# Performance work log

Hardware: AMD Instinct MI355X
Metric: run time of the kernel (lower is better)

Reference implementation:

```python
import jax, jax.numpy as jnp
import numpy as np

B, S, D, H = 2, 2048, 1024, 16
DK = D // H


def setup_inputs() -> dict:
    key = jax.random.key(0)
    ks = jax.random.split(key, 12)
    std = 1.0 / np.sqrt(D)
    inp = {
        "query": jax.random.normal(ks[0], (B, S, D), jnp.float32),
        "key": jax.random.normal(ks[1], (B, S, D), jnp.float32),
        "value": jax.random.normal(ks[2], (B, S, D), jnp.float32),
        # causal decoder mask [B, 1, S, S]; 0 -> masked
        "mask": jnp.broadcast_to(jnp.tril(jnp.ones((S, S), jnp.int32)), (B, 1, S, S)),
        "wq": jax.random.uniform(ks[3], (D, D), jnp.float32, -std, std),
        "bq": jax.random.uniform(ks[4], (D,), jnp.float32, -std, std),
        "wk": jax.random.uniform(ks[5], (D, D), jnp.float32, -std, std),
        "bk": jax.random.uniform(ks[6], (D,), jnp.float32, -std, std),
        "wv": jax.random.uniform(ks[7], (D, D), jnp.float32, -std, std),
        "bv": jax.random.uniform(ks[8], (D,), jnp.float32, -std, std),
        "wo": jax.random.uniform(ks[9], (D, D), jnp.float32, -std, std),
        "bo": jax.random.uniform(ks[10], (D,), jnp.float32, -std, std),
    }
    return inp


def _split_heads(x):
    b, s, _ = x.shape
    return x.reshape(b, s, H, DK).transpose(0, 2, 1, 3)  # [B,H,S,DK]


def reference(query, key, value, mask, wq, bq, wk, bk, wv, bv, wo, bo):
    # nn.Linear: y = x @ W^T + b
    q = _split_heads(query @ wq.T + bq)
    k = _split_heads(key @ wk.T + bk)
    v = _split_heads(value @ wv.T + bv)
    scores = jnp.einsum("bhqd,bhkd->bhqk", q, k) / np.sqrt(DK).astype(np.float32)
    scores = jnp.where(mask == 0, jnp.float32(-1e9), scores)
    attn = jax.nn.softmax(scores, axis=-1)
    # dropout is identity in eval mode
    out = jnp.einsum("bhqk,bhkd->bhqd", attn, v)
    out = out.transpose(0, 2, 1, 3).reshape(query.shape[0], -1, D)
    return out @ wo.T + bo
```

## Files before the change

### kernel.cpp

```cpp
#include <hip/hip_runtime.h>
#include <hip/hip_bf16.h>
#include <cstdint>
#include <cstddef>

#define B_ 2
#define S_ 2048
#define D_ 1024
#define H_ 16
#define DK_ 64

#define AS1 __attribute__((address_space(1)))
#define AS3 __attribute__((address_space(3)))

typedef __attribute__((ext_vector_type(8))) short short8;
typedef __attribute__((ext_vector_type(4))) float f32x4;
typedef __attribute__((ext_vector_type(16))) float f32x16;
typedef __attribute__((ext_vector_type(4))) unsigned short ushort4_t;

__device__ __forceinline__ unsigned short f2bf(float f) {
    union { float f; unsigned u; } x; x.f = f;
    unsigned r = x.u + 0x7fffu + ((x.u >> 16) & 1u);
    return (unsigned short)(r >> 16);
}

__device__ __forceinline__ unsigned pack_bf16(float lo, float hi_) {
    union { __hip_bfloat162 h; unsigned u; } cv;
    cv.h = __float22bfloat162_rn(make_float2(lo, hi_));
    return cv.u;
}

__device__ __forceinline__ float xor32f(float x, int hi) {
#if __has_builtin(__builtin_amdgcn_permlane32_swap)
    unsigned u = __builtin_bit_cast(unsigned, x);
    auto r = __builtin_amdgcn_permlane32_swap(u, u, false, false);
    return __builtin_bit_cast(float, hi ? r[0] : r[1]);
#else
    return __shfl_xor(x, 32);
#endif
}

__device__ __forceinline__ void swap32(unsigned a, unsigned b, unsigned& x, unsigned& y, int hi) {
#if __has_builtin(__builtin_amdgcn_permlane32_swap)
    auto r = __builtin_amdgcn_permlane32_swap(a, b, false, false);
    x = r[0]; y = r[1];
#else
    unsigned pa_ = __shfl_xor(a, 32), pb_ = __shfl_xor(b, 32);
    x = hi ? pb_ : a;
    y = hi ? b : pa_;
#endif
}

__global__ __launch_bounds__(256) void cvt_all(
    const float* __restrict__ q, const float* __restrict__ k, const float* __restrict__ v,
    const float* __restrict__ wq, const float* __restrict__ wk, const float* __restrict__ wv,
    const float* __restrict__ wo,
    unsigned short* __restrict__ xq, unsigned short* __restrict__ xk, unsigned short* __restrict__ xv,
    unsigned short* __restrict__ wqb, unsigned short* __restrict__ wkb, unsigned short* __restrict__ wvb,
    unsigned short* __restrict__ wob) {
    int b = blockIdx.x;
    const float* src; unsigned short* dst; int rel;
    if (b < 6144) {
        int which = b >> 11; rel = b & 2047;
        src = (which == 0) ? q : (which == 1) ? k : v;
        dst = (which == 0) ? xq : (which == 1) ? xk : xv;
    } else {
        int bb = b - 6144; int which = bb >> 9; rel = bb & 511;
        src = (which == 0) ? wq : (which == 1) ? wk : (which == 2) ? wv : wo;
        dst = (which == 0) ? wqb : (which == 1) ? wkb : (which == 2) ? wvb : wob;
    }
    int i = rel * 256 + threadIdx.x;
    const float4* s4 = (const float4*)src;
    float4 a = s4[2 * i], c = s4[2 * i + 1];
    short8 o;
    o[0] = (short)f2bf(a.x); o[1] = (short)f2bf(a.y); o[2] = (short)f2bf(a.z); o[3] = (short)f2bf(a.w);
    o[4] = (short)f2bf(c.x); o[5] = (short)f2bf(c.y); o[6] = (short)f2bf(c.z); o[7] = (short)f2bf(c.w);
    *(short8*)(dst + (size_t)i * 8) = o;
}

template <int OUTMODE>
__device__ __forceinline__ void gemm_body(const unsigned short* __restrict__ Ab,
                                          const unsigned short* __restrict__ Wb,
                                          const float* __restrict__ bias,
                                          void* __restrict__ Cout, float scale,
                                          unsigned short* __restrict__ As0,
                                          unsigned short* __restrict__ As1,
                                          unsigned short* __restrict__ Bs0,
                                          unsigned short* __restrict__ Bs1) {
    constexpr int Kd = 1024;
    const int t = threadIdx.x;
    const int l = t & 63;
    const int l15 = l & 15, l4 = l >> 4;
    const int wid = t >> 6;
    const int wm = wid >> 1, wn = wid & 1;
    const int m0 = (blockIdx.x * 4 + (blockIdx.y & 3)) * 128;
    const int n0 = (blockIdx.y >> 2) * 128;

    f32x4 acc[4][4] = {};

    int ldsoff[4];
    int sgo[4];
#pragma unroll
    for (int p = 0; p < 4; p++) {
        int off = p * 4096 + t * 16;
        int row = off >> 7;
        int slot = (off >> 4) & 7;
        ldsoff[p] = off;
        sgo[p] = row * Kd + (slot ^ (row & 7)) * 8;
    }

#define GLOAD(BUFA, BUFB, K0)                                                         \
    {                                                                                 \
        _Pragma("unroll") for (int p = 0; p < 4; p++)                                 \
            __builtin_amdgcn_global_load_lds(                                         \
                (const AS1 void*)(Ab + (size_t)m0 * Kd + sgo[p] + (K0)),              \
                (AS3 void*)((char*)(BUFA) + ldsoff[p]), 16, 0, 0);                    \
        _Pragma("unroll") for (int p = 0; p < 4; p++)                                 \
            __builtin_amdgcn_global_load_lds(                                         \
                (const AS1 void*)(Wb + (size_t)n0 * Kd + sgo[p] + (K0)),              \
                (AS3 void*)((char*)(BUFB) + ldsoff[p]), 16, 0, 0);                    \
    }

#define GEMMSTEP(CA, CB, NA, NB, K0)                                                  \
    {                                                                                 \
        if ((K0) + 64 < Kd) {                                                         \
            GLOAD(NA, NB, (K0) + 64);                                                 \
            asm volatile("s_waitcnt vmcnt(8)" ::: "memory");                          \
        } else {                                                                      \
            asm volatile("s_waitcnt vmcnt(0)" ::: "memory");                          \
        }                                                                             \
        __builtin_amdgcn_sched_barrier(0);                                            \
        __builtin_amdgcn_s_barrier();                                                 \
        __builtin_amdgcn_sched_barrier(0);                                            \
        _Pragma("unroll") for (int kk = 0; kk < 2; kk++) {                            \
            short8 af[4], bfr[4];                                                     \
            _Pragma("unroll") for (int mi = 0; mi < 4; mi++) {                        \
                int row = wm * 64 + mi * 16 + l15;                                    \
                int slot = kk * 4 + l4;                                               \
                af[mi] = *(const short8*)((const char*)(CA) + row * 128 +             \
                                          ((slot ^ (row & 7)) << 4));                 \
            }                                                                         \
            _Pragma("unroll") for (int ni = 0; ni < 4; ni++) {                        \
                int row = wn * 64 + ni * 16 + l15;                                    \
                int slot = kk * 4 + l4;                                               \
                bfr[ni] = *(const short8*)((const char*)(CB) + row * 128 +            \
                                           ((slot ^ (row & 7)) << 4));                \
            }                                                                         \
            _Pragma("unroll") for (int mi = 0; mi < 4; mi++)                          \
                _Pragma("unroll") for (int ni = 0; ni < 4; ni++)                      \
                    acc[mi][ni] = __builtin_amdgcn_mfma_f32_16x16x32_bf16(            \
                        af[mi], bfr[ni], acc[mi][ni], 0, 0, 0);                       \
        }                                                                             \
        __builtin_amdgcn_s_barrier();                                                 \
        __builtin_amdgcn_sched_barrier(0);                                            \
    }

    GLOAD(As0, Bs0, 0);
    for (int k0 = 0; k0 < Kd; k0 += 128) {
        GEMMSTEP(As0, Bs0, As1, Bs1, k0);
        GEMMSTEP(As1, Bs1, As0, Bs0, k0 + 64);
    }
#undef GEMMSTEP
#undef GLOAD

#pragma unroll
    for (int mi = 0; mi < 4; mi++) {
#pragma unroll
        for (int ni = 0; ni < 4; ni++) {
            int n = n0 + wn * 64 + ni * 16 + l15;
            float bn = bias[n];
            int mb = m0 + wm * 64 + mi * 16 + l4 * 4;
            if constexpr (OUTMODE == 2) {
                int b = mb >> 11, s = mb & 2047, h = n >> 6, dk = n & 63;
                ushort4_t vv;
#pragma unroll
                for (int j = 0; j < 4; j++) vv[j] = f2bf(acc[mi][ni][j] + bn);
                *(ushort4_t*)((unsigned short*)Cout + ((size_t)(b * H_ + h) * DK_ + dk) * S_ + s) = vv;
            } else {
#pragma unroll
                for (int j = 0; j < 4; j++) {
                    float v = (acc[mi][ni][j] + bn) * scale;
                    int m = mb + j;
                    if constexpr (OUTMODE == 0) {
                        int b = m >> 11, s = m & 2047, h = n >> 6, dk = n & 63;
                        ((unsigned short*)Cout)[(((size_t)b * H_ + h) * S_ + s) * DK_ + dk] = f2bf(v);
                    } else {
                        ((float*)Cout)[(size_t)m * D_ + n] = v;
                    }
                }
            }
        }
    }
}

__global__ __launch_bounds__(256, 2) void qkv_gemm(
    const unsigned short* __restrict__ xq, const unsigned short* __restrict__ xk,
    const unsigned short* __restrict__ xv, const unsigned short* __restrict__ wqb,
    const unsigned short* __restrict__ wkb, const unsigned short* __restrict__ wvb,
    const float* __restrict__ bq, const float* __restrict__ bk, const float* __restrict__ bv,
    unsigned short* __restrict__ qo, unsigned short* __restrict__ ko, unsigned short* __restrict__ vto,
    float qscale) {
    __shared__ unsigned short As[2][128 * 64];
    __shared__ unsigned short Bs[2][128 * 64];
    int z = blockIdx.z;
    if (z == 2) {
        gemm_body<2>(xv, wvb, bv, vto, 1.0f, As[0], As[1], Bs[0], Bs[1]);
    } else if (z == 0) {
        gemm_body<0>(xq, wqb, bq, qo, qscale, As[0], As[1], Bs[0], Bs[1]);
    } else {
        gemm_body<0>(xk, wkb, bk, ko, 1.0f, As[0], As[1], Bs[0], Bs[1]);
    }
}

__global__ __launch_bounds__(256, 2) void out_gemm(const unsigned short* __restrict__ Aa,
                                                   const unsigned short* __restrict__ Wo,
                                                   const float* __restrict__ bo,
                                                   float* __restrict__ out) {
    __shared__ unsigned short As[2][128 * 64];
    __shared__ unsigned short Bs[2][128 * 64];
    gemm_body<1>(Aa, Wo, bo, out, 1.0f, As[0], As[1], Bs[0], Bs[1]);
}

union AttnSm {
    unsigned short kv[2][2][128 * 64];
    struct { float obuf[2][2][32][64]; float lArr[2][4][32]; } m;
};

__device__ __forceinline__ void attn_compute(const short8 kf[4], const short8 vf[4],
                                             const short8 qf[4], int lq, int hi, bool diag,
                                             f32x16& o0, f32x16& o1, float& l_run) {
    f32x16 sT = {};
    __builtin_amdgcn_s_setprio(1);
#pragma unroll
    for (int c = 0; c < 4; c++)
        sT = __builtin_amdgcn_mfma_f32_32x32x16_bf16(kf[c], qf[c], sT, 0, 0, 0);
    __builtin_amdgcn_s_setprio(0);

    float e[16];
#pragma unroll
    for (int r = 0; r < 16; r++) e[r] = exp2f(sT[r]);
    if (diag) {
#pragma unroll
        for (int r = 0; r < 16; r++) {
            int kvl = (r & 3) + 8 * (r >> 2) + 4 * hi;
            e[r] = (kvl <= lq) ? e[r] : 0.0f;
        }
    }

    float s8[8];
#pragma unroll
    for (int r = 0; r < 8; r++) s8[r] = e[2 * r] + e[2 * r + 1];
#pragma unroll
    for (int r = 0; r < 4; r++) s8[r] = s8[r] + s8[r + 4];
    float ps = (s8[0] + s8[1]) + (s8[2] + s8[3]);
    ps += xor32f(ps, hi);
    l_run += ps;

    unsigned OW[8];
#pragma unroll
    for (int w = 0; w < 8; w++) OW[w] = pack_bf16(e[2 * w], e[2 * w + 1]);

    union { unsigned u[4]; short8 s; } pa0, pa1;
    swap32(OW[0], OW[2], pa0.u[0], pa0.u[2], hi);
    swap32(OW[1], OW[3], pa0.u[1], pa0.u[3], hi);
    swap32(OW[4], OW[6], pa1.u[0], pa1.u[2], hi);
    swap32(OW[5], OW[7], pa1.u[1], pa1.u[3], hi);

    __builtin_amdgcn_s_setprio(1);
    o0 = __builtin_amdgcn_mfma_f32_32x32x16_bf16(pa0.s, vf[0], o0, 0, 0, 0);
    o1 = __builtin_amdgcn_mfma_f32_32x32x16_bf16(pa0.s, vf[1], o1, 0, 0, 0);
    o0 = __builtin_amdgcn_mfma_f32_32x32x16_bf16(pa1.s, vf[2], o0, 0, 0, 0);
    o1 = __builtin_amdgcn_mfma_f32_32x32x16_bf16(pa1.s, vf[3], o1, 0, 0, 0);
    __builtin_amdgcn_s_setprio(0);
}

__global__ __launch_bounds__(512, 4) void attn_kernel(const unsigned short* __restrict__ Q,
                                                      const unsigned short* __restrict__ Kk,
                                                      const unsigned short* __restrict__ Vt,
                                                      unsigned short* __restrict__ Aout) {
    __shared__ AttnSm sm;

    const int t_ = threadIdx.x;
    const int l = t_ & 63;
    const int w = t_ >> 6;
    const int qsub = w >> 2, kvw = w & 3;
    const int lq = l & 31, hi = l >> 5;

    const int bid = blockIdx.x;
    const int xcd = bid & 7, j = bid >> 3;
    const int bh = xcd * 4 + (j >> 5);
    const int bq = 31 - (j & 31);
    const int wq0 = bq * 64;
    const int qi = 2 * bq + qsub;
    const int T = ((2 * bq + 1) >> 2) + 1;

    const unsigned short* Qh = Q + (size_t)bh * S_ * DK_;
    const unsigned short* Kh = Kk + (size_t)bh * S_ * DK_;
    const unsigned short* Vth = Vt + (size_t)bh * DK_ * S_;

    short8 qf[4];
    const unsigned short* qrow = Qh + (size_t)(wq0 + qsub * 32 + lq) * DK_ + hi * 8;
#pragma unroll
    for (int c = 0; c < 4; c++) qf[c] = *(const short8*)(qrow + 16 * c);

    f32x16 o0 = {}, o1 = {};
    float l_run = 0.f;

    const int lr = kvw * 32 + lq;
    unsigned kaddr[4], vaddr[4];
#pragma unroll
    for (int c = 0; c < 4; c++)
        kaddr[c] = (unsigned)(lr * 128 + (((2 * c + hi) ^ (lr & 7)) << 4));
#pragma unroll
    for (int c = 0; c < 2; c++) {
        unsigned sl = (unsigned)(((kvw * 4 + 2 * c + hi) ^ (lq & 15)) << 4);
        vaddr[2 * c] = (unsigned)(lq * 256) + sl;
        vaddr[2 * c + 1] = (unsigned)((lq + 32) * 256) + sl;
    }

    const int off0 = t_ * 16, off1 = 8192 + t_ * 16;
    int ldsoff[2] = {off0, off1};
    const char* kgp[2];
    const char* vgp[2];
#pragma unroll
    for (int p = 0; p < 2; p++) {
        int off = (p == 0) ? off0 : off1;
        int rk = off >> 7, slk = (off >> 4) & 7;
        kgp[p] = (const char*)Kh + rk * 128 + ((slk ^ (rk & 7)) << 4);
        int rv = off >> 8, slv = (off >> 4) & 15;
        vgp[p] = (const char*)Vth + (size_t)rv * (S_ * 2) + ((slv ^ (rv & 15)) << 4);
    }

#define STAGE(BUF)                                                                      \
    {                                                                                   \
        _Pragma("unroll") for (int p = 0; p < 2; p++) {                                 \
            __builtin_amdgcn_global_load_lds((const AS1 void*)kgp[p],                   \
                (AS3 void*)((char*)sm.kv[BUF][0] + ldsoff[p]), 16, 0, 0);               \
            kgp[p] += 128 * DK_ * 2;                          \
        }                                                                               \
        _Pragma("unroll") for (int p = 0; p < 2; p++) {                                 \
            __builtin_amdgcn_global_load_lds((const AS1 void*)vgp[p],                   \
                (AS3 void*)((char*)sm.kv[BUF][1] + ldsoff[p]), 16, 0, 0);               \
            vgp[p] += 128 * 2;                     \
        }                                                                               \
    }

#define TILE_STEP(BUF, T_IDX)                                                           \
    {                                                                                   \
        if ((T_IDX) + 1 < T) { asm volatile("s_waitcnt vmcnt(4)" ::: "memory"); }       \
        else                 { asm volatile("s_waitcnt vmcnt(0)" ::: "memory"); }       \
        __builtin_amdgcn_sched_barrier(0);                                              \
        __builtin_amdgcn_s_barrier();                                                   \
        __builtin_amdgcn_sched_barrier(0);                                              \
        const int sidx = 4 * (T_IDX) + kvw;                                             \
        if (sidx <= qi) {                                                               \
            short8 kf[4], vf[4];                                                        \
            const char* Kbuf = (const char*)sm.kv[BUF][0];                              \
            const char* Vbuf = (const char*)sm.kv[BUF][1];                              \
            _Pragma("unroll") for (int c = 0; c < 4; c++)                               \
                kf[c] = *(const short8*)(Kbuf + kaddr[c]);                              \
            _Pragma("unroll") for (int c = 0; c < 4; c++)                               \
                vf[c] = *(const short8*)(Vbuf + vaddr[c]);                              \
            attn_compute(kf, vf, qf, lq, hi, sidx == qi, o0, o1, l_run);                \
        }                                                                               \
        asm volatile("s_waitcnt lgkmcnt(0)" ::: "memory");                              \
        __builtin_amdgcn_sched_barrier(0);                                              \
        __builtin_amdgcn_s_barrier();                                                   \
        __builtin_amdgcn_sched_barrier(0);                                              \
        if ((T_IDX) + 2 < T) STAGE(BUF);                                                \
    }

    STAGE(0);
    STAGE(1);

    for (int t = 0; t < T; t += 2) {
        TILE_STEP(0, t);
        if (t + 1 < T) TILE_STEP(1, t + 1);
    }
#undef TILE_STEP
#undef STAGE

    float(&obuf)[2][2][32][64] = sm.m.obuf;
    float(&lArr)[2][4][32] = sm.m.lArr;
    if (hi == 0) lArr[qsub][kvw][lq] = l_run;

    if (kvw < 2) {
#pragma unroll
        for (int r = 0; r < 16; r++) {
            int qrw = (r & 3) + 8 * (r >> 2) + 4 * hi;
            obuf[qsub][kvw][qrw][lq] = o0[r];
            obuf[qsub][kvw][qrw][lq + 32] = o1[r];
        }
    }
    __syncthreads();
    if (kvw >= 2) {
#pragma unroll
        for (int r = 0; r < 16; r++) {
            int qrw = (r & 3) + 8 * (r >> 2) + 4 * hi;
            obuf[qsub][kvw - 2][qrw][lq] += o0[r];
            obuf[qsub][kvw - 2][qrw][lq + 32] += o1[r];
        }
    }
    __syncthreads();

    const int b = bh >> 4, h = bh & 15;
    const int row = (w & 3) * 8 + (l >> 3);
    const int dk0 = (l & 7) * 8;
    float ls = lArr[qsub][0][row] + lArr[qsub][1][row] + lArr[qsub][2][row] + lArr[qsub][3][row];
    float inv = 1.0f / ls;
    short8 ov;
#pragma unroll
    for (int jj = 0; jj < 8; jj++) {
        float s = obuf[qsub][0][row][dk0 + jj] + obuf[qsub][1][row][dk0 + jj];
        ov[jj] = (short)f2bf(s * inv);
    }
    unsigned short* orow = Aout + ((size_t)b * S_ + (wq0 + qsub * 32 + row)) * D_ + h * 64 + dk0;
    *(short8*)orow = ov;
}

extern "C" void kernel_launch(void* const* d_in, const int* in_sizes, int n_in,
                              void* d_out, int out_size, void* d_ws, size_t ws_size,
                              hipStream_t stream) {
    const float* query = (const float*)d_in[0];
    const float* key = (const float*)d_in[1];
    const float* value = (const float*)d_in[2];
    const float* wq = (const float*)d_in[4];
    const float* bq = (const float*)d_in[5];
    const float* wk = (const float*)d_in[6];
    const float* bk = (const float*)d_in[7];
    const float* wv = (const float*)d_in[8];
    const float* bv = (const float*)d_in[9];
    const float* wo = (const float*)d_in[10];
    const float* bo = (const float*)d_in[11];

    const size_t NX = (size_t)B_ * S_ * D_;
    const size_t NW = (size_t)D_ * D_;
    char* p = (char*)d_ws;
    unsigned short* xq = (unsigned short*)p; p += NX * 2;
    unsigned short* xk = (unsigned short*)p; p += NX * 2;
    unsigned short* xv = (unsigned short*)p; p += NX * 2;
    unsigned short* wqb = (unsigned short*)p; p += NW * 2;
    unsigned short* wkb = (unsigned short*)p; p += NW * 2;
    unsigned short* wvb = (unsigned short*)p; p += NW * 2;
    unsigned short* wob = (unsigned short*)p; p += NW * 2;
    unsigned short* qb = (unsigned short*)p; p += NX * 2;
    unsigned short* kb = (unsigned short*)p; p += NX * 2;
    unsigned short* vtb = (unsigned short*)p; p += NX * 2;
    unsigned short* ab = (unsigned short*)p; p += NX * 2;

    cvt_all<<<dim3(8192), dim3(256), 0, stream>>>(query, key, value, wq, wk, wv, wo,
                                                  xq, xk, xv, wqb, wkb, wvb, wob);

    const float qscale = 0.125f * 1.4426950408889634f;
    qkv_gemm<<<dim3(8, 32, 3), dim3(256), 0, stream>>>(xq, xk, xv, wqb, wkb, wvb,
                                                       bq, bk, bv, qb, kb, vtb, qscale);
    attn_kernel<<<dim3(1024), dim3(512), 0, stream>>>(qb, kb, vtb, ab);
    out_gemm<<<dim3(8, 32), dim3(256), 0, stream>>>(ab, wob, bo, (float*)d_out);
}
```

Measured before the change: 119.7 us.

## Restructure attention blocks to 128 queries with 64-key tiles and 2-way KV split

Each attention block now covers 128 query rows using 4 query-subgroups × 2 KV-split waves instead of 64 rows with 2×4. K/V tiles shrink from 128 to 64 keys, which halves LDS per block, and launch bounds are raised to allow 8 blocks/CU. The grid halves to 512 blocks. Each K/V tile is reused by more queries, and the cross-wave reduction is cheaper. The cost is fewer blocks for load balance on causal work and more loop iterations with smaller tiles.

```diff
diff --git a/kernel.cpp b/kernel.cpp
--- a/kernel.cpp
+++ b/kernel.cpp
@@ -221,8 +221,8 @@
 }
 
 union AttnSm {
-    unsigned short kv[2][2][128 * 64];
-    struct { float obuf[2][2][32][64]; float lArr[2][4][32]; } m;
+    unsigned short kv[2][2][64 * 64];
+    struct { float obuf[4][32][64]; float lArr[4][2][32]; } m;
 };
 
 __device__ __forceinline__ void attn_compute(const short8 kf[4], const short8 vf[4],
@@ -273,7 +273,7 @@
     __builtin_amdgcn_s_setprio(0);
 }
 
-__global__ __launch_bounds__(512, 4) void attn_kernel(const unsigned short* __restrict__ Q,
+__global__ __launch_bounds__(512, 8) void attn_kernel(const unsigned short* __restrict__ Q,
                                                       const unsigned short* __restrict__ Kk,
                                                       const unsigned short* __restrict__ Vt,
                                                       unsigned short* __restrict__ Aout) {
@@ -282,16 +282,16 @@
     const int t_ = threadIdx.x;
     const int l = t_ & 63;
     const int w = t_ >> 6;
-    const int qsub = w >> 2, kvw = w & 3;
+    const int qsub = w >> 1, kvw = w & 1;
     const int lq = l & 31, hi = l >> 5;
 
     const int bid = blockIdx.x;
     const int xcd = bid & 7, j = bid >> 3;
-    const int bh = xcd * 4 + (j >> 5);
-    const int bq = 31 - (j & 31);
-    const int wq0 = bq * 64;
-    const int qi = 2 * bq + qsub;
-    const int T = ((2 * bq + 1) >> 2) + 1;
+    const int bh = xcd * 4 + (j >> 4);
+    const int qb = 15 - (j & 15);
+    const int wq0 = qb * 128;
+    const int qi = 4 * qb + qsub;
+    const int T = 2 * qb + 2;
 
     const unsigned short* Qh = Q + (size_t)bh * S_ * DK_;
     const unsigned short* Kh = Kk + (size_t)bh * S_ * DK_;
@@ -312,46 +312,36 @@
         kaddr[c] = (unsigned)(lr * 128 + (((2 * c + hi) ^ (lr & 7)) << 4));
 #pragma unroll
     for (int c = 0; c < 2; c++) {
-        unsigned sl = (unsigned)(((kvw * 4 + 2 * c + hi) ^ (lq & 15)) << 4);
-        vaddr[2 * c] = (unsigned)(lq * 256) + sl;
-        vaddr[2 * c + 1] = (unsigned)((lq + 32) * 256) + sl;
-    }
-
-    const int off0 = t_ * 16, off1 = 8192 + t_ * 16;
-    int ldsoff[2] = {off0, off1};
-    const char* kgp[2];
-    const char* vgp[2];
-#pragma unroll
-    for (int p = 0; p < 2; p++) {
-        int off = (p == 0) ? off0 : off1;
-        int rk = off >> 7, slk = (off >> 4) & 7;
-        kgp[p] = (const char*)Kh + rk * 128 + ((slk ^ (rk & 7)) << 4);
-        int rv = off >> 8, slv = (off >> 4) & 15;
-        vgp[p] = (const char*)Vth + (size_t)rv * (S_ * 2) + ((slv ^ (rv & 15)) << 4);
-    }
+        unsigned sl = (unsigned)(((kvw * 4 + 2 * c + hi) ^ (lq & 7)) << 4);
+        vaddr[2 * c] = (unsigned)(lq * 128) + sl;
+        vaddr[2 * c + 1] = (unsigned)((lq + 32) * 128) + sl;
+    }
+
+    const int ldso = t_ * 16;
+    {
+    }
+    const int rs = ldso >> 7, sls = (ldso >> 4) & 7;
+    const char* kgp = (const char*)Kh + rs * 128 + ((sls ^ (rs & 7)) << 4);
+    const char* vgp = (const char*)Vth + (size_t)rs * (S_ * 2) + ((sls ^ (rs & 7)) << 4);
 
 #define STAGE(BUF)                                                                      \
     {                                                                                   \
-        _Pragma("unroll") for (int p = 0; p < 2; p++) {                                 \
-            __builtin_amdgcn_global_load_lds((const AS1 void*)kgp[p],                   \
-                (AS3 void*)((char*)sm.kv[BUF][0] + ldsoff[p]), 16, 0, 0);               \
-            kgp[p] += 128 * DK_ * 2;                          \
-        }                                                                               \
-        _Pragma("unroll") for (int p = 0; p < 2; p++) {                                 \
-            __builtin_amdgcn_global_load_lds((const AS1 void*)vgp[p],                   \
-                (AS3 void*)((char*)sm.kv[BUF][1] + ldsoff[p]), 16, 0, 0);               \
-            vgp[p] += 128 * 2;                     \
-        }                                                                               \
+        __builtin_amdgcn_global_load_lds((const AS1 void*)kgp,                          \
+            (AS3 void*)((char*)sm.kv[BUF][0] + ldso), 16, 0, 0);                        \
+        kgp += 64 * DK_ * 2;                                   \
+        __builtin_amdgcn_global_load_lds((const AS1 void*)vgp,                          \
+            (AS3 void*)((char*)sm.kv[BUF][1] + ldso), 16, 0, 0);                        \
+        vgp += 64 * 2;                             \
     }
 
 #define TILE_STEP(BUF, T_IDX)                                                           \
     {                                                                                   \
-        if ((T_IDX) + 1 < T) { asm volatile("s_waitcnt vmcnt(4)" ::: "memory"); }       \
+        if ((T_IDX) + 1 < T) { asm volatile("s_waitcnt vmcnt(2)" ::: "memory"); }       \
         else                 { asm volatile("s_waitcnt vmcnt(0)" ::: "memory"); }       \
         __builtin_amdgcn_sched_barrier(0);                                              \
         __builtin_amdgcn_s_barrier();                                                   \
         __builtin_amdgcn_sched_barrier(0);                                              \
-        const int sidx = 4 * (T_IDX) + kvw;                                             \
+        const int sidx = 2 * (T_IDX) + kvw;                                             \
         if (sidx <= qi) {                                                               \
             short8 kf[4], vf[4];                                                        \
             const char* Kbuf = (const char*)sm.kv[BUF][0];                              \
@@ -374,47 +364,48 @@
 
     for (int t = 0; t < T; t += 2) {
         TILE_STEP(0, t);
-        if (t + 1 < T) TILE_STEP(1, t + 1);
+        TILE_STEP(1, t + 1);
     }
 #undef TILE_STEP
 #undef STAGE
 
-    float(&obuf)[2][2][32][64] = sm.m.obuf;
-    float(&lArr)[2][4][32] = sm.m.lArr;
+    float(&obuf)[4][32][64] = sm.m.obuf;
+    float(&lArr)[4][2][32] = sm.m.lArr;
     if (hi == 0) lArr[qsub][kvw][lq] = l_run;
 
-    if (kvw < 2) {
+    if (kvw == 0) {
 #pragma unroll
         for (int r = 0; r < 16; r++) {
             int qrw = (r & 3) + 8 * (r >> 2) + 4 * hi;
-            obuf[qsub][kvw][qrw][lq] = o0[r];
-            obuf[qsub][kvw][qrw][lq + 32] = o1[r];
+            obuf[qsub][qrw][lq] = o0[r];
+            obuf[qsub][qrw][lq + 32] = o1[r];
         }
     }
     __syncthreads();
-    if (kvw >= 2) {
+    if (kvw == 1) {
 #pragma unroll
         for (int r = 0; r < 16; r++) {
             int qrw = (r & 3) + 8 * (r >> 2) + 4 * hi;
-            obuf[qsub][kvw - 2][qrw][lq] += o0[r];
-            obuf[qsub][kvw - 2][qrw][lq + 32] += o1[r];
+            obuf[qsub][qrw][lq] += o0[r];
+            obuf[qsub][qrw][lq + 32] += o1[r];
         }
     }
     __syncthreads();
 
     const int b = bh >> 4, h = bh & 15;
-    const int row = (w & 3) * 8 + (l >> 3);
-    const int dk0 = (l & 7) * 8;
-    float ls = lArr[qsub][0][row] + lArr[qsub][1][row] + lArr[qsub][2][row] + lArr[qsub][3][row];
+    const int row = (w & 1) * 16 + (l >> 2);
+    const int dk0 = (l & 3) * 16;
+    float ls = lArr[qsub][0][row] + lArr[qsub][1][row];
     float inv = 1.0f / ls;
-    short8 ov;
+    short8 ov0, ov1;
 #pragma unroll
     for (int jj = 0; jj < 8; jj++) {
-        float s = obuf[qsub][0][row][dk0 + jj] + obuf[qsub][1][row][dk0 + jj];
-        ov[jj] = (short)f2bf(s * inv);
+        ov0[jj] = (short)f2bf(obuf[qsub][row][dk0 + jj] * inv);
+        ov1[jj] = (short)f2bf(obuf[qsub][row][dk0 + 8 + jj] * inv);
     }
     unsigned short* orow = Aout + ((size_t)b * S_ + (wq0 + qsub * 32 + row)) * D_ + h * 64 + dk0;
-    *(short8*)orow = ov;
+    *(short8*)orow = ov0;
+    *(short8*)(orow + 8) = ov1;
 }
 
 extern "C" void kernel_launch(void* const* d_in, const int* in_sizes, int n_in,
@@ -453,6 +444,6 @@
     const float qscale = 0.125f * 1.4426950408889634f;
     qkv_gemm<<<dim3(8, 32, 3), dim3(256), 0, stream>>>(xq, xk, xv, wqb, wkb, wvb,
                                                        bq, bk, bv, qb, kb, vtb, qscale);
-    attn_kernel<<<dim3(1024), dim3(512), 0, stream>>>(qb, kb, vtb, ab);
+    attn_kernel<<<dim3(512), dim3(512), 0, stream>>>(qb, kb, vtb, ab);
     out_gemm<<<dim3(8, 32), dim3(256), 0, stream>>>(ab, wob, bo, (float*)d_out);
 }
```

Result: slower. 416.4 us (+247.7%).

## Store V in chunked fragment layout and load V directly from global memory

Applied to the files above, without the earlier changes.

The QKV GEMM now writes transposed V in a blocked layout of 32-key chunks per dk row, so each attention wave can read its V MFMA fragments straight from global memory with contiguous 16-byte loads. V is no longer staged through LDS, which halves the shared-memory buffer and the async copy traffic per tile, and the vmcnt wait threshold is adjusted to match. In exchange, V reads go through L2/global inside the compute path with nothing to hide their latency, which may stall the MFMA loop.

```diff
diff --git a/kernel.cpp b/kernel.cpp
--- a/kernel.cpp
+++ b/kernel.cpp
@@ -174,7 +174,8 @@
                 ushort4_t vv;
 #pragma unroll
                 for (int j = 0; j < 4; j++) vv[j] = f2bf(acc[mi][ni][j] + bn);
-                *(ushort4_t*)((unsigned short*)Cout + ((size_t)(b * H_ + h) * DK_ + dk) * S_ + s) = vv;
+                size_t idx = (((size_t)(b * H_ + h) * 64 + (s >> 5)) * 64 + dk) * 32 + (s & 31);
+                *(ushort4_t*)((unsigned short*)Cout + idx) = vv;
             } else {
 #pragma unroll
                 for (int j = 0; j < 4; j++) {
@@ -221,7 +222,7 @@
 }
 
 union AttnSm {
-    unsigned short kv[2][2][128 * 64];
+    unsigned short kv[2][128 * 64];
     struct { float obuf[2][2][32][64]; float lArr[2][4][32]; } m;
 };
 
@@ -295,7 +296,7 @@
 
     const unsigned short* Qh = Q + (size_t)bh * S_ * DK_;
     const unsigned short* Kh = Kk + (size_t)bh * S_ * DK_;
-    const unsigned short* Vth = Vt + (size_t)bh * DK_ * S_;
+    const unsigned short* Vtc = Vt + (size_t)bh * DK_ * S_;
 
     short8 qf[4];
     const unsigned short* qrow = Qh + (size_t)(wq0 + qsub * 32 + lq) * DK_ + hi * 8;
@@ -306,47 +307,35 @@
     float l_run = 0.f;
 
     const int lr = kvw * 32 + lq;
-    unsigned kaddr[4], vaddr[4];
+    unsigned kaddr[4];
 #pragma unroll
     for (int c = 0; c < 4; c++)
         kaddr[c] = (unsigned)(lr * 128 + (((2 * c + hi) ^ (lr & 7)) << 4));
-#pragma unroll
-    for (int c = 0; c < 2; c++) {
-        unsigned sl = (unsigned)(((kvw * 4 + 2 * c + hi) ^ (lq & 15)) << 4);
-        vaddr[2 * c] = (unsigned)(lq * 256) + sl;
-        vaddr[2 * c + 1] = (unsigned)((lq + 32) * 256) + sl;
-    }
+
+    const unsigned short* vp = Vtc + lq * 32 + hi * 8;
 
     const int off0 = t_ * 16, off1 = 8192 + t_ * 16;
     int ldsoff[2] = {off0, off1};
     const char* kgp[2];
-    const char* vgp[2];
 #pragma unroll
     for (int p = 0; p < 2; p++) {
         int off = (p == 0) ? off0 : off1;
         int rk = off >> 7, slk = (off >> 4) & 7;
         kgp[p] = (const char*)Kh + rk * 128 + ((slk ^ (rk & 7)) << 4);
-        int rv = off >> 8, slv = (off >> 4) & 15;
-        vgp[p] = (const char*)Vth + (size_t)rv * (S_ * 2) + ((slv ^ (rv & 15)) << 4);
     }
 
 #define STAGE(BUF)                                                                      \
     {                                                                                   \
         _Pragma("unroll") for (int p = 0; p < 2; p++) {                                 \
             __builtin_amdgcn_global_load_lds((const AS1 void*)kgp[p],                   \
-                (AS3 void*)((char*)sm.kv[BUF][0] + ldsoff[p]), 16, 0, 0);               \
+                (AS3 void*)((char*)sm.kv[BUF] + ldsoff[p]), 16, 0, 0);                  \
             kgp[p] += 128 * DK_ * 2;                          \
         }                                                                               \
-        _Pragma("unroll") for (int p = 0; p < 2; p++) {                                 \
-            __builtin_amdgcn_global_load_lds((const AS1 void*)vgp[p],                   \
-                (AS3 void*)((char*)sm.kv[BUF][1] + ldsoff[p]), 16, 0, 0);               \
-            vgp[p] += 128 * 2;                     \
-        }                                                                               \
     }
 
 #define TILE_STEP(BUF, T_IDX)                                                           \
     {                                                                                   \
-        if ((T_IDX) + 1 < T) { asm volatile("s_waitcnt vmcnt(4)" ::: "memory"); }       \
+        if ((T_IDX) + 1 < T) { asm volatile("s_waitcnt vmcnt(2)" ::: "memory"); }       \
         else                 { asm volatile("s_waitcnt vmcnt(0)" ::: "memory"); }       \
         __builtin_amdgcn_sched_barrier(0);                                              \
         __builtin_amdgcn_s_barrier();                                                   \
@@ -354,12 +343,15 @@
         const int sidx = 4 * (T_IDX) + kvw;                                             \
         if (sidx <= qi) {                                                               \
             short8 kf[4], vf[4];                                                        \
-            const char* Kbuf = (const char*)sm.kv[BUF][0];                              \
-            const char* Vbuf = (const char*)sm.kv[BUF][1];                              \
+                 \
+            const unsigned short* vb_ = vp + (size_t)(sidx)*2048;                       \
+            vf[0] = *(const short8*)(vb_);                                              \
+            vf[2] = *(const short8*)(vb_ + 16);                                         \
+            vf[1] = *(const short8*)(vb_ + 1024);                                       \
+            vf[3] = *(const short8*)(vb_ + 1024 + 16);                                  \
+            const char* Kbuf = (const char*)sm.kv[BUF];                                 \
             _Pragma("unroll") for (int c = 0; c < 4; c++)                               \
                 kf[c] = *(const short8*)(Kbuf + kaddr[c]);                              \
-            _Pragma("unroll") for (int c = 0; c < 4; c++)                               \
-                vf[c] = *(const short8*)(Vbuf + vaddr[c]);                              \
             attn_compute(kf, vf, qf, lq, hi, sidx == qi, o0, o1, l_run);                \
         }                                                                               \
         asm volatile("s_waitcnt lgkmcnt(0)" ::: "memory");                              \
```

After: 124.0 us. +3.5%, slower.
